# Optimization experiments

Measured on AMD Instinct MI355X. Metric: run time of the kernel, lower is better.

Reference implementation:

```python
import jax, jax.numpy as jnp
import numpy as np

MAX_ITERS = 256  # matches init_kwargs max_iters


def setup_inputs() -> dict:
    key = jax.random.key(0)
    k1, k2 = jax.random.split(key)
    H = W = 4096
    # classic Mandelbrot viewing window
    c_real = jax.random.uniform(k1, (H, W), jnp.float32, -2.0, 0.5)
    c_imag = jax.random.uniform(k2, (H, W), jnp.float32, -1.25, 1.25)
    return {"c_real": c_real, "c_imag": c_imag}


def reference(c_real, c_imag):
    # z starts at c (NOT zero), as in the torch module
    zr0 = c_real
    zi0 = c_imag
    active0 = jnp.ones(c_real.shape, dtype=bool)
    counts0 = jnp.full(c_real.shape, float(MAX_ITERS), dtype=c_real.dtype)

    def body(step, state):
        zr, zi, active, counts = state
        escaped_now = active & (zr * zr + zi * zi >= 4.0)
        counts = jnp.where(escaped_now, step.astype(counts.dtype), counts)
        active = active & ~escaped_now
        # torch loop only updates z for step < max_iters
        do_update = active & (step < MAX_ITERS)
        next_real = zr * zr - zi * zi + c_real
        next_imag = 2.0 * zr * zi + c_imag
        zr = jnp.where(do_update, next_real, zr)
        zi = jnp.where(do_update, next_imag, zi)
        return (zr, zi, active, counts)

    _, _, _, counts = jax.lax.fori_loop(
        0, MAX_ITERS + 1, body, (zr0, zi0, active0, counts0)
    )
    return counts
```

## Files before the change

kernel.cpp:

```cpp
#include <hip/hip_runtime.h>


#define MAX_ITERS 256

typedef __attribute__((ext_vector_type(2))) float f32x2;
typedef __attribute__((ext_vector_type(4))) float f32x4;

__device__ __forceinline__ float mul32(float a, float b) {
    float d; asm("v_mul_f32 %0, %1, %2" : "=v"(d) : "v"(a), "v"(b)); return d;
}
__device__ __forceinline__ float add32(float a, float b) {
    float d; asm("v_add_f32 %0, %1, %2" : "=v"(d) : "v"(a), "v"(b)); return d;
}
__device__ __forceinline__ float fma32(float a, float b, float c) {
    float d; asm("v_fma_f32 %0, %1, %2, %3" : "=v"(d) : "v"(a), "v"(b), "v"(c)); return d;
}
__device__ __forceinline__ float fma32_negc(float a, float b, float c) {
    float d; asm("v_fma_f32 %0, %1, %2, -%3" : "=v"(d) : "v"(a), "v"(b), "v"(c)); return d;
}

__device__ __forceinline__ void iter_checks(float cr, float ci,
                                            float& zr, float& zi,
                                            float& act, float& cnt, int nchecks)
{
    #pragma unroll 8
    for (int s = 0; s < nchecks; ++s) {
        const float zi2 = mul32(zi, zi);
        const float mag = fma32(zr, zr, zi2);
        act = (mag < 4.0f) ? act : 0.0f;
        cnt = cnt + act;
        const float t   = fma32_negc(zr, zr, zi2);
        const float nr  = add32(t, cr);
        const float t2  = add32(zr, zr);
        zi = fma32(t2, zi, ci);
        zr = nr;
    }
}

__device__ __forceinline__ void zstep2(const f32x2 cr, const f32x2 ci,
                                       f32x2& zr, f32x2& zi, f32x2& mag)
{
    f32x2 s, t, u;
    asm("v_pk_mul_f32 %0, %5, %5\n\t"
        "v_pk_fma_f32 %1, %4, %4, %0\n\t"
        "v_pk_fma_f32 %2, %4, %4, %0 neg_lo:[0,0,1] neg_hi:[0,0,1]\n\t"
        "v_pk_add_f32 %3, %4, %4\n\t"
        "v_pk_add_f32 %4, %2, %6\n\t"
        "v_pk_fma_f32 %5, %3, %5, %7"
        : "=&v"(s), "=&v"(mag), "=&v"(t), "=&v"(u), "+v"(zr), "+v"(zi)
        : "v"(cr), "v"(ci));
}

__device__ __forceinline__ void check4(
    const f32x2 crA, const f32x2 ciA, f32x2& zrA, f32x2& ziA,
    const f32x2 crB, const f32x2 ciB, f32x2& zrB, f32x2& ziB,
    float& act0, float& act1, float& act2, float& act3,
    float& cnt0, float& cnt1, float& cnt2, float& cnt3)
{
    f32x2 magA, magB;
    zstep2(crA, ciA, zrA, ziA, magA);
    zstep2(crB, ciB, zrB, ziB, magB);
    act0 = (magA.x < 4.0f) ? act0 : 0.0f;  cnt0 += act0;
    act1 = (magA.y < 4.0f) ? act1 : 0.0f;  cnt1 += act1;
    act2 = (magB.x < 4.0f) ? act2 : 0.0f;  cnt2 += act2;
    act3 = (magB.y < 4.0f) ? act3 : 0.0f;  cnt3 += act3;
}

__device__ __forceinline__ int lane_id() {
    return __builtin_amdgcn_mbcnt_hi(~0u, __builtin_amdgcn_mbcnt_lo(~0u, 0));
}

__device__ __forceinline__ bool in_shortcut(float cr, float ci) {
    const float xq = cr - 0.25f;
    const float q  = xq * xq + ci * ci;
    const bool in_card = (q * (q + xq) - 0.25f * ci * ci) < -1e-3f;
    const float xb = cr + 1.0f;
    const bool in_bulb = (xb * xb + ci * ci) < (0.0625f - 1e-3f);
    return in_card | in_bulb;
}

__global__ void zero_ctrs(unsigned char* ws) {
    if (threadIdx.x < 64)
        *(unsigned*)(ws + (size_t)threadIdx.x * 64u) = 0u;
}

__global__ __launch_bounds__(256) void mandel_stage_a_q(
    const float* __restrict__ c_real, const float* __restrict__ c_imag,
    float* __restrict__ out, unsigned char* __restrict__ ws,
    unsigned seg_cap, int n)
{
    const int tq = blockIdx.x * blockDim.x + threadIdx.x;
    const int p0 = tq << 2;
    if (p0 >= n) return;

    if (p0 + 3 >= n) {
        for (int j = 0; j < 4 && p0 + j < n; ++j) {
            const float cr = c_real[p0 + j], ci = c_imag[p0 + j];
            if (in_shortcut(cr, ci)) { out[p0 + j] = 256.0f; continue; }
            float zr = cr, zi = ci, act = 1.0f, cnt = 0.0f;
            iter_checks(cr, ci, zr, zi, act, cnt, MAX_ITERS);
            out[p0 + j] = cnt;
        }
        return;
    }

    const f32x4 cr4 = *(const f32x4*)(c_real + p0);
    const f32x4 ci4 = *(const f32x4*)(c_imag + p0);
    const f32x2 crA = {cr4.x, cr4.y}, ciA = {ci4.x, ci4.y};
    const f32x2 crB = {cr4.z, cr4.w}, ciB = {ci4.z, ci4.w};
    const bool sc0 = in_shortcut(cr4.x, ci4.x);
    const bool sc1 = in_shortcut(cr4.y, ci4.y);
    const bool sc2 = in_shortcut(cr4.z, ci4.z);
    const bool sc3 = in_shortcut(cr4.w, ci4.w);

    f32x2 zrA = crA, ziA = ciA, zrB = crB, ziB = ciB;
    float act0 = 1.0f, act1 = 1.0f, act2 = 1.0f, act3 = 1.0f;
    float cnt0 = 0.0f, cnt1 = 0.0f, cnt2 = 0.0f, cnt3 = 0.0f;
    #pragma unroll
    for (int s = 0; s < 16; ++s)
        check4(crA, ciA, zrA, ziA, crB, ciB, zrB, ziB,
               act0, act1, act2, act3, cnt0, cnt1, cnt2, cnt3);

    const bool sv0 = (!sc0) && (act0 != 0.0f);
    const bool sv1 = (!sc1) && (act1 != 0.0f);
    const bool sv2 = (!sc2) && (act2 != 0.0f);
    const bool sv3 = (!sc3) && (act3 != 0.0f);

    const unsigned long long m0 = __ballot(sv0);
    const unsigned long long m1 = __ballot(sv1);
    const unsigned long long m2 = __ballot(sv2);
    const unsigned long long m3 = __ballot(sv3);
    const unsigned long long any = m0 | m1 | m2 | m3;
    if (any != 0ull) {
        const int lane = lane_id();
        const int leader = (int)__ffsll(any) - 1;
        const int seg = blockIdx.x & 63;
        unsigned* ctr = (unsigned*)(ws + (size_t)seg * 64u);
        const unsigned c0 = (unsigned)__popcll(m0);
        const unsigned c1 = (unsigned)__popcll(m1);
        const unsigned c2 = (unsigned)__popcll(m2);
        const unsigned c3 = (unsigned)__popcll(m3);
        unsigned base = 0u;
        if (lane == leader) base = atomicAdd(ctr, c0 + c1 + c2 + c3);
        base = (unsigned)__shfl((int)base, leader, 64);
        float4* qf = (float4*)(ws + 4096);
        int*    qi = (int*)(ws + 4096 + (size_t)seg_cap * 64u * 16u);
        const unsigned long long below = (1ull << lane) - 1ull;
        const size_t segbase = (size_t)seg * seg_cap;
        const unsigned pre1 = c0, pre2 = c0 + c1, pre3 = c0 + c1 + c2;

        float zrv[4] = {zrA.x, zrA.y, zrB.x, zrB.y};
        float ziv[4] = {ziA.x, ziA.y, ziB.x, ziB.y};
        float crv[4] = {cr4.x, cr4.y, cr4.z, cr4.w};
        float civ[4] = {ci4.x, ci4.y, ci4.z, ci4.w};
        float cnv[4] = {cnt0, cnt1, cnt2, cnt3};
        const bool svv[4] = {sv0, sv1, sv2, sv3};
        const unsigned prev[4] = {0u, pre1, pre2, pre3};
        const unsigned long long mv[4] = {m0, m1, m2, m3};
        #pragma unroll
        for (int j = 0; j < 4; ++j) {
            if (!svv[j]) continue;
            const unsigned slot = base + prev[j] +
                (unsigned)__popcll(mv[j] & below);
            if (slot < seg_cap) {
                qf[segbase + slot] = make_float4(zrv[j], ziv[j], crv[j], civ[j]);
                qi[segbase + slot] = p0 + j;
            } else {
                float zrs = zrv[j], zis = ziv[j], as = 1.0f, cs = cnv[j];
                iter_checks(crv[j], civ[j], zrs, zis, as, cs, 240);
                out[p0 + j] = cs;
            }
        }
    }
    if (!sv0) out[p0 + 0] = sc0 ? 256.0f : cnt0;
    if (!sv1) out[p0 + 1] = sc1 ? 256.0f : cnt1;
    if (!sv2) out[p0 + 2] = sc2 ? 256.0f : cnt2;
    if (!sv3) out[p0 + 3] = sc3 ? 256.0f : cnt3;
}

__global__ __launch_bounds__(256) void mandel_stage_b_q(
    float* __restrict__ out, const unsigned char* __restrict__ ws,
    unsigned seg_cap, int blocks_per_seg)
{
    const int seg = (int)(blockIdx.x & 63u);
    const int grp = (int)(blockIdx.x >> 6);
    const unsigned cnt_s = *(const unsigned*)(ws + (size_t)seg * 64u);
    const unsigned nq = (cnt_s < seg_cap) ? cnt_s : seg_cap;
    const unsigned q = (nq + 3u) >> 2;
    const unsigned stride = (unsigned)blocks_per_seg * 256u;
    const float4* qf = (const float4*)(ws + 4096);
    const int*    qi = (const int*)(ws + 4096 + (size_t)seg_cap * 64u * 16u);
    const size_t segbase = (size_t)seg * seg_cap;

    for (unsigned k = (unsigned)grp * 256u + threadIdx.x; k < q; k += stride) {
        const unsigned i1 = k + q, i2 = k + 2u * q, i3 = k + 3u * q;
        const bool v1 = (i1 < nq), v2 = (i2 < nq), v3 = (i3 < nq);
        const float4 r0 = qf[segbase + k];
        const float4 r1 = v1 ? qf[segbase + i1] : r0;
        const float4 r2 = v2 ? qf[segbase + i2] : r0;
        const float4 r3 = v3 ? qf[segbase + i3] : r0;
        const int idx0 = qi[segbase + k];
        const int idx1 = v1 ? qi[segbase + i1] : -1;
        const int idx2 = v2 ? qi[segbase + i2] : -1;
        const int idx3 = v3 ? qi[segbase + i3] : -1;

        f32x2 zrA = {r0.x, r1.x}, ziA = {r0.y, r1.y};
        f32x2 crA = {r0.z, r1.z}, ciA = {r0.w, r1.w};
        f32x2 zrB = {r2.x, r3.x}, ziB = {r2.y, r3.y};
        f32x2 crB = {r2.z, r3.z}, ciB = {r2.w, r3.w};
        float act0 = 1.0f, act1 = v1 ? 1.0f : 0.0f;
        float act2 = v2 ? 1.0f : 0.0f, act3 = v3 ? 1.0f : 0.0f;
        float cnt0 = 16.0f, cnt1 = 16.0f, cnt2 = 16.0f, cnt3 = 16.0f;
        #pragma unroll 8
        for (int s = 0; s < 240; ++s)
            check4(crA, ciA, zrA, ziA, crB, ciB, zrB, ziB,
                   act0, act1, act2, act3, cnt0, cnt1, cnt2, cnt3);
        out[idx0] = cnt0;
        if (v1) out[idx1] = cnt1;
        if (v2) out[idx2] = cnt2;
        if (v3) out[idx3] = cnt3;
    }
}

__global__ __launch_bounds__(256) void mandel_mono(
    const float* __restrict__ c_real, const float* __restrict__ c_imag,
    float* __restrict__ out, int n)
{
    int i = blockIdx.x * blockDim.x + threadIdx.x;
    if (i >= n) return;
    const float cr = c_real[i], ci = c_imag[i];
    float zr = cr, zi = ci, act = 1.0f, cnt = 0.0f;
    iter_checks(cr, ci, zr, zi, act, cnt, MAX_ITERS);
    out[i] = cnt;
}

extern "C" void kernel_launch(void* const* d_in, const int* in_sizes, int n_in,
                              void* d_out, int out_size, void* d_ws, size_t ws_size,
                              hipStream_t stream)
{
    const float* c_real = (const float*)d_in[0];
    const float* c_imag = (const float*)d_in[1];
    float* out = (float*)d_out;
    const int n = in_sizes[0];
    const int block = 256;

    unsigned char* ws = (unsigned char*)d_ws;
    const size_t avail = (ws_size > 4096) ? (ws_size - 4096) : 0;
    const unsigned seg_cap = (unsigned)(avail / (64u * 20u));

    if (seg_cap < 8192u) {
        const int gridA = (n + block - 1) / block;
        mandel_mono<<<gridA, block, 0, stream>>>(c_real, c_imag, out, n);
        return;
    }

    zero_ctrs<<<1, 64, 0, stream>>>(ws);

    const int nquads = (n + 3) / 4;
    const int gridA = (nquads + block - 1) / block;
    mandel_stage_a_q<<<gridA, block, 0, stream>>>(c_real, c_imag, out,
                                                  ws, seg_cap, n);
    const int bps = 32;
    mandel_stage_b_q<<<64 * bps, block, 0, stream>>>(out, ws, seg_cap, bps);
}
```

Measured before the change: 237.6 us.

## Split escape-time queue into multi-stage compaction passes with ping-pong buffers

Replaces the single stage-B pass, which runs 240 iterations on every surviving point, with three strip kernels of 40, 80 and 120 iterations. After each strip, points still active are recompacted into a ping-pong queue using wave ballots and per-segment atomic counters. This cuts divergence waste, since each wave in later stages holds only long-lived points. The cost is two extra launches, extra queue reads and writes, and atomics. Counter zeroing also moves from a tiny kernel to hipMemsetAsync.

```diff
diff --git a/kernel.cpp b/kernel.cpp
--- a/kernel.cpp
+++ b/kernel.cpp
@@ -79,20 +79,11 @@
     return in_card | in_bulb;
 }
 
-__global__ void zero_ctrs(unsigned char* ws) {
-    if (threadIdx.x < 64)
-        *(unsigned*)(ws + (size_t)threadIdx.x * 64u) = 0u;
-}
-
-__global__ __launch_bounds__(256) void mandel_stage_a_q(
+__device__ __forceinline__ void phaseA_quad(
     const float* __restrict__ c_real, const float* __restrict__ c_imag,
     float* __restrict__ out, unsigned char* __restrict__ ws,
-    unsigned seg_cap, int n)
-{
-    const int tq = blockIdx.x * blockDim.x + threadIdx.x;
-    const int p0 = tq << 2;
-    if (p0 >= n) return;
-
+    unsigned seg_cap, int n, int p0, int seg)
+{
     if (p0 + 3 >= n) {
         for (int j = 0; j < 4 && p0 + j < n; ++j) {
             const float cr = c_real[p0 + j], ci = c_imag[p0 + j];
@@ -134,20 +125,18 @@
     if (any != 0ull) {
         const int lane = lane_id();
         const int leader = (int)__ffsll(any) - 1;
-        const int seg = blockIdx.x & 63;
         unsigned* ctr = (unsigned*)(ws + (size_t)seg * 64u);
         const unsigned c0 = (unsigned)__popcll(m0);
         const unsigned c1 = (unsigned)__popcll(m1);
         const unsigned c2 = (unsigned)__popcll(m2);
-        const unsigned c3 = (unsigned)__popcll(m3);
         unsigned base = 0u;
-        if (lane == leader) base = atomicAdd(ctr, c0 + c1 + c2 + c3);
+        if (lane == leader)
+            base = atomicAdd(ctr, c0 + c1 + c2 + (unsigned)__popcll(m3));
         base = (unsigned)__shfl((int)base, leader, 64);
         float4* qf = (float4*)(ws + 4096);
         int*    qi = (int*)(ws + 4096 + (size_t)seg_cap * 64u * 16u);
         const unsigned long long below = (1ull << lane) - 1ull;
         const size_t segbase = (size_t)seg * seg_cap;
-        const unsigned pre1 = c0, pre2 = c0 + c1, pre3 = c0 + c1 + c2;
 
         float zrv[4] = {zrA.x, zrA.y, zrB.x, zrB.y};
         float ziv[4] = {ziA.x, ziA.y, ziB.x, ziB.y};
@@ -155,7 +144,7 @@
         float civ[4] = {ci4.x, ci4.y, ci4.z, ci4.w};
         float cnv[4] = {cnt0, cnt1, cnt2, cnt3};
         const bool svv[4] = {sv0, sv1, sv2, sv3};
-        const unsigned prev[4] = {0u, pre1, pre2, pre3};
+        const unsigned prev[4] = {0u, c0, c0 + c1, c0 + c1 + c2};
         const unsigned long long mv[4] = {m0, m1, m2, m3};
         #pragma unroll
         for (int j = 0; j < 4; ++j) {
@@ -178,31 +167,34 @@
     if (!sv3) out[p0 + 3] = sc3 ? 256.0f : cnt3;
 }
 
-__global__ __launch_bounds__(256) void mandel_stage_b_q(
-    float* __restrict__ out, const unsigned char* __restrict__ ws,
-    unsigned seg_cap, int blocks_per_seg)
-{
-    const int seg = (int)(blockIdx.x & 63u);
-    const int grp = (int)(blockIdx.x >> 6);
-    const unsigned cnt_s = *(const unsigned*)(ws + (size_t)seg * 64u);
+template <int NCHECKS, int START, bool HAS_DST>
+__device__ __forceinline__ void strip_phase(
+    float* __restrict__ out, unsigned char* __restrict__ ws,
+    const float4* __restrict__ srcF, const int* __restrict__ srcI,
+    float4* __restrict__ dstF, int* __restrict__ dstI,
+    int src_ctr, int dst_ctr, unsigned seg_cap,
+    int seg, int grp, int blocks_per_seg)
+{
+    const unsigned cnt_s = __hip_atomic_load(
+        (const unsigned*)(ws + (size_t)seg * 64u + (size_t)src_ctr * 4u),
+        __ATOMIC_RELAXED, __HIP_MEMORY_SCOPE_AGENT);
     const unsigned nq = (cnt_s < seg_cap) ? cnt_s : seg_cap;
     const unsigned q = (nq + 3u) >> 2;
     const unsigned stride = (unsigned)blocks_per_seg * 256u;
-    const float4* qf = (const float4*)(ws + 4096);
-    const int*    qi = (const int*)(ws + 4096 + (size_t)seg_cap * 64u * 16u);
     const size_t segbase = (size_t)seg * seg_cap;
+    const int lane = lane_id();
 
     for (unsigned k = (unsigned)grp * 256u + threadIdx.x; k < q; k += stride) {
         const unsigned i1 = k + q, i2 = k + 2u * q, i3 = k + 3u * q;
         const bool v1 = (i1 < nq), v2 = (i2 < nq), v3 = (i3 < nq);
-        const float4 r0 = qf[segbase + k];
-        const float4 r1 = v1 ? qf[segbase + i1] : r0;
-        const float4 r2 = v2 ? qf[segbase + i2] : r0;
-        const float4 r3 = v3 ? qf[segbase + i3] : r0;
-        const int idx0 = qi[segbase + k];
-        const int idx1 = v1 ? qi[segbase + i1] : -1;
-        const int idx2 = v2 ? qi[segbase + i2] : -1;
-        const int idx3 = v3 ? qi[segbase + i3] : -1;
+        const float4 r0 = srcF[segbase + k];
+        const float4 r1 = v1 ? srcF[segbase + i1] : r0;
+        const float4 r2 = v2 ? srcF[segbase + i2] : r0;
+        const float4 r3 = v3 ? srcF[segbase + i3] : r0;
+        const int idx0 = srcI[segbase + k];
+        const int idx1 = v1 ? srcI[segbase + i1] : -1;
+        const int idx2 = v2 ? srcI[segbase + i2] : -1;
+        const int idx3 = v3 ? srcI[segbase + i3] : -1;
 
         f32x2 zrA = {r0.x, r1.x}, ziA = {r0.y, r1.y};
         f32x2 crA = {r0.z, r1.z}, ciA = {r0.w, r1.w};
@@ -210,16 +202,96 @@
         f32x2 crB = {r2.z, r3.z}, ciB = {r2.w, r3.w};
         float act0 = 1.0f, act1 = v1 ? 1.0f : 0.0f;
         float act2 = v2 ? 1.0f : 0.0f, act3 = v3 ? 1.0f : 0.0f;
-        float cnt0 = 16.0f, cnt1 = 16.0f, cnt2 = 16.0f, cnt3 = 16.0f;
+        float cnt0 = (float)START, cnt1 = (float)START;
+        float cnt2 = (float)START, cnt3 = (float)START;
         #pragma unroll 8
-        for (int s = 0; s < 240; ++s)
+        for (int s = 0; s < NCHECKS; ++s)
             check4(crA, ciA, zrA, ziA, crB, ciB, zrB, ziB,
                    act0, act1, act2, act3, cnt0, cnt1, cnt2, cnt3);
-        out[idx0] = cnt0;
-        if (v1) out[idx1] = cnt1;
-        if (v2) out[idx2] = cnt2;
-        if (v3) out[idx3] = cnt3;
-    }
+
+        if (HAS_DST) {
+            const bool sv0 = (act0 != 0.0f);
+            const bool sv1 = (act1 != 0.0f);
+            const bool sv2 = (act2 != 0.0f);
+            const bool sv3 = (act3 != 0.0f);
+            const unsigned long long m0 = __ballot(sv0);
+            const unsigned long long m1 = __ballot(sv1);
+            const unsigned long long m2 = __ballot(sv2);
+            const unsigned long long m3 = __ballot(sv3);
+            const unsigned long long any = m0 | m1 | m2 | m3;
+            if (any != 0ull) {
+                const int leader = (int)__ffsll(any) - 1;
+                unsigned* ctr = (unsigned*)(ws + (size_t)seg * 64u
+                                               + (size_t)dst_ctr * 4u);
+                const unsigned c0 = (unsigned)__popcll(m0);
+                const unsigned c1 = (unsigned)__popcll(m1);
+                const unsigned c2 = (unsigned)__popcll(m2);
+                unsigned base = 0u;
+                if (lane == leader)
+                    base = atomicAdd(ctr, c0 + c1 + c2 + (unsigned)__popcll(m3));
+                base = (unsigned)__shfl((int)base, leader, 64);
+                const unsigned long long below = (1ull << lane) - 1ull;
+
+                float zrv[4] = {zrA.x, zrA.y, zrB.x, zrB.y};
+                float ziv[4] = {ziA.x, ziA.y, ziB.x, ziB.y};
+                float crv[4] = {crA.x, crA.y, crB.x, crB.y};
+                float civ[4] = {ciA.x, ciA.y, ciB.x, ciB.y};
+                float cnv[4] = {cnt0, cnt1, cnt2, cnt3};
+                const int  idxv[4] = {idx0, idx1, idx2, idx3};
+                const bool svv[4] = {sv0, sv1, sv2, sv3};
+                const unsigned prev[4] = {0u, c0, c0 + c1, c0 + c1 + c2};
+                const unsigned long long mv[4] = {m0, m1, m2, m3};
+                #pragma unroll
+                for (int j = 0; j < 4; ++j) {
+                    if (!svv[j]) continue;
+                    const unsigned slot = base + prev[j] +
+                        (unsigned)__popcll(mv[j] & below);
+                    if (slot < seg_cap) {
+                        dstF[segbase + slot] =
+                            make_float4(zrv[j], ziv[j], crv[j], civ[j]);
+                        dstI[segbase + slot] = idxv[j];
+                    } else {
+                        float zrs = zrv[j], zis = ziv[j], as = 1.0f, cs = cnv[j];
+                        iter_checks(crv[j], civ[j], zrs, zis, as, cs,
+                                    256 - START - NCHECKS);
+                        out[idxv[j]] = cs;
+                    }
+                }
+            }
+            if (!sv0) out[idx0] = cnt0;
+            if (v1 && !sv1) out[idx1] = cnt1;
+            if (v2 && !sv2) out[idx2] = cnt2;
+            if (v3 && !sv3) out[idx3] = cnt3;
+        } else {
+            out[idx0] = cnt0;
+            if (v1) out[idx1] = cnt1;
+            if (v2) out[idx2] = cnt2;
+            if (v3) out[idx3] = cnt3;
+        }
+    }
+}
+
+__global__ __launch_bounds__(256) void mandel_stage_a_q(
+    const float* __restrict__ c_real, const float* __restrict__ c_imag,
+    float* __restrict__ out, unsigned char* __restrict__ ws,
+    unsigned seg_cap, int n)
+{
+    const int tq = blockIdx.x * blockDim.x + threadIdx.x;
+    const int p0 = tq << 2;
+    if (p0 >= n) return;
+    phaseA_quad(c_real, c_imag, out, ws, seg_cap, n, p0, blockIdx.x & 63);
+}
+
+template <int NCHECKS, int START, bool HAS_DST>
+__global__ __launch_bounds__(256) void mandel_strip_q(
+    float* __restrict__ out, unsigned char* __restrict__ ws,
+    const float4* __restrict__ srcF, const int* __restrict__ srcI,
+    float4* __restrict__ dstF, int* __restrict__ dstI,
+    int src_ctr, int dst_ctr, unsigned seg_cap, int blocks_per_seg)
+{
+    strip_phase<NCHECKS, START, HAS_DST>(
+        out, ws, srcF, srcI, dstF, dstI, src_ctr, dst_ctr, seg_cap,
+        (int)(blockIdx.x & 63u), (int)(blockIdx.x >> 6), blocks_per_seg);
 }
 
 __global__ __launch_bounds__(256) void mandel_mono(
@@ -246,20 +318,44 @@
 
     unsigned char* ws = (unsigned char*)d_ws;
     const size_t avail = (ws_size > 4096) ? (ws_size - 4096) : 0;
-    const unsigned seg_cap = (unsigned)(avail / (64u * 20u));
-
-    if (seg_cap < 8192u) {
+    const unsigned seg_cap1 = (unsigned)(avail / (64u * 20u));
+    const unsigned seg_cap2 = (unsigned)(avail / (64u * 20u * 2u));
+
+    if (seg_cap1 < 8192u) {
         const int gridA = (n + block - 1) / block;
         mandel_mono<<<gridA, block, 0, stream>>>(c_real, c_imag, out, n);
         return;
     }
 
-    zero_ctrs<<<1, 64, 0, stream>>>(ws);
+    hipMemsetAsync(ws, 0, 4096, stream);
 
     const int nquads = (n + 3) / 4;
     const int gridA = (nquads + block - 1) / block;
+
+    if (seg_cap2 >= 33000u) {
+        const unsigned sc = seg_cap2;
+        float4* q0f = (float4*)(ws + 4096);
+        int*    q0i = (int*)(ws + 4096 + (size_t)sc * 64u * 16u);
+        float4* q1f = (float4*)(ws + 4096 + (size_t)sc * 64u * 20u);
+        int*    q1i = (int*)(ws + 4096 + (size_t)sc * 64u * 20u
+                                       + (size_t)sc * 64u * 16u);
+
+        mandel_stage_a_q<<<gridA, block, 0, stream>>>(c_real, c_imag, out,
+                                                      ws, sc, n);
+        mandel_strip_q<40, 16, true><<<64 * 32, block, 0, stream>>>(
+            out, ws, q0f, q0i, q1f, q1i, 0, 1, sc, 32);
+        mandel_strip_q<80, 56, true><<<64 * 16, block, 0, stream>>>(
+            out, ws, q1f, q1i, q0f, q0i, 1, 2, sc, 16);
+        mandel_strip_q<120, 136, false><<<64 * 16, block, 0, stream>>>(
+            out, ws, q0f, q0i, (float4*)nullptr, (int*)nullptr, 2, 0, sc, 16);
+        return;
+    }
+
     mandel_stage_a_q<<<gridA, block, 0, stream>>>(c_real, c_imag, out,
-                                                  ws, seg_cap, n);
-    const int bps = 32;
-    mandel_stage_b_q<<<64 * bps, block, 0, stream>>>(out, ws, seg_cap, bps);
-}
+                                                  ws, seg_cap1, n);
+    mandel_strip_q<240, 16, false><<<64 * 32, block, 0, stream>>>(
+        out, ws,
+        (const float4*)(ws + 4096),
+        (const int*)(ws + 4096 + (size_t)seg_cap1 * 64u * 16u),
+        (float4*)nullptr, (int*)nullptr, 0, 0, seg_cap1, 32);
+}
```

Measured after the change: 239.0 us. About the same (+0.6%).

## Fuse screening and survivor stages into one persistent kernel with LDS pool

Applied to the files above, without the earlier changes.

Replaces the three-kernel pipeline (counter zeroing, 16-iteration screening with global-memory survivor queues, separate 240-iteration drain kernel) with a single persistent kernel. Each block stages survivors in a shared-memory pool and drains 1024 at a time once the pool fills, then drains the remainder at the end. This removes global queue traffic, global atomics and the extra launches. In exchange it adds block-wide barriers on every group and can leave load imbalance at the tail, since each block's leftover pool is processed by that block alone.

```diff
diff --git a/kernel.cpp b/kernel.cpp
--- a/kernel.cpp
+++ b/kernel.cpp
@@ -2,6 +2,8 @@
 
 
 #define MAX_ITERS 256
+#define POOL_CAP 1280
+#define DRAIN_AT 1024
 
 typedef __attribute__((ext_vector_type(2))) float f32x2;
 typedef __attribute__((ext_vector_type(4))) float f32x4;
@@ -79,159 +81,170 @@
     return in_card | in_bulb;
 }
 
-__global__ void zero_ctrs(unsigned char* ws) {
-    if (threadIdx.x < 64)
-        *(unsigned*)(ws + (size_t)threadIdx.x * 64u) = 0u;
-}
-
-__global__ __launch_bounds__(256) void mandel_stage_a_q(
-    const float* __restrict__ c_real, const float* __restrict__ c_imag,
-    float* __restrict__ out, unsigned char* __restrict__ ws,
-    unsigned seg_cap, int n)
-{
-    const int tq = blockIdx.x * blockDim.x + threadIdx.x;
-    const int p0 = tq << 2;
-    if (p0 >= n) return;
-
-    if (p0 + 3 >= n) {
-        for (int j = 0; j < 4 && p0 + j < n; ++j) {
-            const float cr = c_real[p0 + j], ci = c_imag[p0 + j];
-            if (in_shortcut(cr, ci)) { out[p0 + j] = 256.0f; continue; }
-            float zr = cr, zi = ci, act = 1.0f, cnt = 0.0f;
-            iter_checks(cr, ci, zr, zi, act, cnt, MAX_ITERS);
-            out[p0 + j] = cnt;
-        }
-        return;
-    }
-
-    const f32x4 cr4 = *(const f32x4*)(c_real + p0);
-    const f32x4 ci4 = *(const f32x4*)(c_imag + p0);
-    const f32x2 crA = {cr4.x, cr4.y}, ciA = {ci4.x, ci4.y};
-    const f32x2 crB = {cr4.z, cr4.w}, ciB = {ci4.z, ci4.w};
-    const bool sc0 = in_shortcut(cr4.x, ci4.x);
-    const bool sc1 = in_shortcut(cr4.y, ci4.y);
-    const bool sc2 = in_shortcut(cr4.z, ci4.z);
-    const bool sc3 = in_shortcut(cr4.w, ci4.w);
-
-    f32x2 zrA = crA, ziA = ciA, zrB = crB, ziB = ciB;
-    float act0 = 1.0f, act1 = 1.0f, act2 = 1.0f, act3 = 1.0f;
-    float cnt0 = 0.0f, cnt1 = 0.0f, cnt2 = 0.0f, cnt3 = 0.0f;
-    #pragma unroll
-    for (int s = 0; s < 16; ++s)
+__device__ __forceinline__ void drain4(
+    const float4 r0, const float4 r1, const float4 r2, const float4 r3,
+    const bool v0, const bool v1, const bool v2, const bool v3,
+    const int i0, const int i1, const int i2, const int i3,
+    float* __restrict__ out)
+{
+    f32x2 zrA; zrA.x = r0.x; zrA.y = r1.x;
+    f32x2 ziA; ziA.x = r0.y; ziA.y = r1.y;
+    f32x2 crA; crA.x = r0.z; crA.y = r1.z;
+    f32x2 ciA; ciA.x = r0.w; ciA.y = r1.w;
+    f32x2 zrB; zrB.x = r2.x; zrB.y = r3.x;
+    f32x2 ziB; ziB.x = r2.y; ziB.y = r3.y;
+    f32x2 crB; crB.x = r2.z; crB.y = r3.z;
+    f32x2 ciB; ciB.x = r2.w; ciB.y = r3.w;
+    float act0 = v0 ? 1.0f : 0.0f, act1 = v1 ? 1.0f : 0.0f;
+    float act2 = v2 ? 1.0f : 0.0f, act3 = v3 ? 1.0f : 0.0f;
+    float cnt0 = 16.0f, cnt1 = 16.0f, cnt2 = 16.0f, cnt3 = 16.0f;
+    #pragma unroll 8
+    for (int s = 0; s < 240; ++s)
         check4(crA, ciA, zrA, ziA, crB, ciB, zrB, ziB,
                act0, act1, act2, act3, cnt0, cnt1, cnt2, cnt3);
-
-    const bool sv0 = (!sc0) && (act0 != 0.0f);
-    const bool sv1 = (!sc1) && (act1 != 0.0f);
-    const bool sv2 = (!sc2) && (act2 != 0.0f);
-    const bool sv3 = (!sc3) && (act3 != 0.0f);
-
-    const unsigned long long m0 = __ballot(sv0);
-    const unsigned long long m1 = __ballot(sv1);
-    const unsigned long long m2 = __ballot(sv2);
-    const unsigned long long m3 = __ballot(sv3);
-    const unsigned long long any = m0 | m1 | m2 | m3;
-    if (any != 0ull) {
-        const int lane = lane_id();
-        const int leader = (int)__ffsll(any) - 1;
-        const int seg = blockIdx.x & 63;
-        unsigned* ctr = (unsigned*)(ws + (size_t)seg * 64u);
-        const unsigned c0 = (unsigned)__popcll(m0);
-        const unsigned c1 = (unsigned)__popcll(m1);
-        const unsigned c2 = (unsigned)__popcll(m2);
-        const unsigned c3 = (unsigned)__popcll(m3);
-        unsigned base = 0u;
-        if (lane == leader) base = atomicAdd(ctr, c0 + c1 + c2 + c3);
-        base = (unsigned)__shfl((int)base, leader, 64);
-        float4* qf = (float4*)(ws + 4096);
-        int*    qi = (int*)(ws + 4096 + (size_t)seg_cap * 64u * 16u);
-        const unsigned long long below = (1ull << lane) - 1ull;
-        const size_t segbase = (size_t)seg * seg_cap;
-        const unsigned pre1 = c0, pre2 = c0 + c1, pre3 = c0 + c1 + c2;
-
-        float zrv[4] = {zrA.x, zrA.y, zrB.x, zrB.y};
-        float ziv[4] = {ziA.x, ziA.y, ziB.x, ziB.y};
-        float crv[4] = {cr4.x, cr4.y, cr4.z, cr4.w};
-        float civ[4] = {ci4.x, ci4.y, ci4.z, ci4.w};
-        float cnv[4] = {cnt0, cnt1, cnt2, cnt3};
-        const bool svv[4] = {sv0, sv1, sv2, sv3};
-        const unsigned prev[4] = {0u, pre1, pre2, pre3};
-        const unsigned long long mv[4] = {m0, m1, m2, m3};
-        #pragma unroll
-        for (int j = 0; j < 4; ++j) {
-            if (!svv[j]) continue;
-            const unsigned slot = base + prev[j] +
-                (unsigned)__popcll(mv[j] & below);
-            if (slot < seg_cap) {
-                qf[segbase + slot] = make_float4(zrv[j], ziv[j], crv[j], civ[j]);
-                qi[segbase + slot] = p0 + j;
+    if (v0) out[i0] = cnt0;
+    if (v1) out[i1] = cnt1;
+    if (v2) out[i2] = cnt2;
+    if (v3) out[i3] = cnt3;
+}
+
+__global__ __launch_bounds__(256) void mandel_fused(
+    const float* __restrict__ c_real, const float* __restrict__ c_imag,
+    float* __restrict__ out, int n)
+{
+    __shared__ float4 poolF[POOL_CAP];
+    __shared__ int    poolI[POOL_CAP];
+    __shared__ int    pool_cnt;
+
+    const int tid = (int)threadIdx.x;
+    const int lane = lane_id();
+    if (tid == 0) pool_cnt = 0;
+    __syncthreads();
+
+    const int ngroups = (n + 1023) >> 10;
+
+    for (int g = (int)blockIdx.x; g < ngroups; g += (int)gridDim.x) {
+        const int p0 = (g << 10) + (tid << 2);
+        if (p0 < n) {
+            if (p0 + 3 >= n) {
+                for (int j = 0; j < 4 && p0 + j < n; ++j) {
+                    const float cr = c_real[p0 + j], ci = c_imag[p0 + j];
+                    if (in_shortcut(cr, ci)) { out[p0 + j] = 256.0f; continue; }
+                    float zr = cr, zi = ci, act = 1.0f, cnt = 0.0f;
+                    iter_checks(cr, ci, zr, zi, act, cnt, MAX_ITERS);
+                    out[p0 + j] = cnt;
+                }
             } else {
-                float zrs = zrv[j], zis = ziv[j], as = 1.0f, cs = cnv[j];
-                iter_checks(crv[j], civ[j], zrs, zis, as, cs, 240);
-                out[p0 + j] = cs;
+                const f32x4 cr4 = *(const f32x4*)(c_real + p0);
+                const f32x4 ci4 = *(const f32x4*)(c_imag + p0);
+                f32x2 crA; crA.x = cr4.x; crA.y = cr4.y;
+                f32x2 ciA; ciA.x = ci4.x; ciA.y = ci4.y;
+                f32x2 crB; crB.x = cr4.z; crB.y = cr4.w;
+                f32x2 ciB; ciB.x = ci4.z; ciB.y = ci4.w;
+                const bool sc0 = in_shortcut(cr4.x, ci4.x);
+                const bool sc1 = in_shortcut(cr4.y, ci4.y);
+                const bool sc2 = in_shortcut(cr4.z, ci4.z);
+                const bool sc3 = in_shortcut(cr4.w, ci4.w);
+
+                f32x2 zrA = crA, ziA = ciA, zrB = crB, ziB = ciB;
+                float act0 = 1.0f, act1 = 1.0f, act2 = 1.0f, act3 = 1.0f;
+                float cnt0 = 0.0f, cnt1 = 0.0f, cnt2 = 0.0f, cnt3 = 0.0f;
+                #pragma unroll
+                for (int s = 0; s < 16; ++s)
+                    check4(crA, ciA, zrA, ziA, crB, ciB, zrB, ziB,
+                           act0, act1, act2, act3, cnt0, cnt1, cnt2, cnt3);
+
+                const bool sv0 = (!sc0) && (act0 != 0.0f);
+                const bool sv1 = (!sc1) && (act1 != 0.0f);
+                const bool sv2 = (!sc2) && (act2 != 0.0f);
+                const bool sv3 = (!sc3) && (act3 != 0.0f);
+
+                const unsigned long long m0 = __ballot(sv0);
+                const unsigned long long m1 = __ballot(sv1);
+                const unsigned long long m2 = __ballot(sv2);
+                const unsigned long long m3 = __ballot(sv3);
+                const unsigned long long any = m0 | m1 | m2 | m3;
+                if (any != 0ull) {
+                    const int leader = (int)__ffsll(any) - 1;
+                    const unsigned c0 = (unsigned)__popcll(m0);
+                    const unsigned c1 = (unsigned)__popcll(m1);
+                    const unsigned c2 = (unsigned)__popcll(m2);
+                    int base_i = 0;
+                    if (lane == leader)
+                        base_i = atomicAdd(&pool_cnt,
+                            (int)(c0 + c1 + c2 + (unsigned)__popcll(m3)));
+                    const unsigned base =
+                        (unsigned)__shfl(base_i, leader, 64);
+                    const unsigned long long below = (1ull << lane) - 1ull;
+
+                    const float zrv[4] = {zrA.x, zrA.y, zrB.x, zrB.y};
+                    const float ziv[4] = {ziA.x, ziA.y, ziB.x, ziB.y};
+                    const float crv[4] = {cr4.x, cr4.y, cr4.z, cr4.w};
+                    const float civ[4] = {ci4.x, ci4.y, ci4.z, ci4.w};
+                    const float cnv[4] = {cnt0, cnt1, cnt2, cnt3};
+                    const bool svv[4] = {sv0, sv1, sv2, sv3};
+                    const unsigned prev[4] = {0u, c0, c0 + c1, c0 + c1 + c2};
+                    const unsigned long long mv[4] = {m0, m1, m2, m3};
+                    #pragma unroll
+                    for (int j = 0; j < 4; ++j) {
+                        if (!svv[j]) continue;
+                        const unsigned slot = base + prev[j] +
+                            (unsigned)__popcll(mv[j] & below);
+                        if (slot < POOL_CAP) {
+                            poolF[slot] = make_float4(zrv[j], ziv[j],
+                                                      crv[j], civ[j]);
+                            poolI[slot] = p0 + j;
+                        } else {
+                            float zrs = zrv[j], zis = ziv[j];
+                            float as = 1.0f, cs = cnv[j];
+                            iter_checks(crv[j], civ[j], zrs, zis, as, cs, 240);
+                            out[p0 + j] = cs;
+                        }
+                    }
+                }
+                if (!sv0) out[p0 + 0] = sc0 ? 256.0f : cnt0;
+                if (!sv1) out[p0 + 1] = sc1 ? 256.0f : cnt1;
+                if (!sv2) out[p0 + 2] = sc2 ? 256.0f : cnt2;
+                if (!sv3) out[p0 + 3] = sc3 ? 256.0f : cnt3;
             }
         }
+        __syncthreads();
+        const int cnt = pool_cnt;
+        if (cnt >= DRAIN_AT) {
+            const float4 r0 = poolF[tid];
+            const float4 r1 = poolF[tid + 256];
+            const float4 r2 = poolF[tid + 512];
+            const float4 r3 = poolF[tid + 768];
+            const int i0 = poolI[tid];
+            const int i1 = poolI[tid + 256];
+            const int i2 = poolI[tid + 512];
+            const int i3 = poolI[tid + 768];
+            __syncthreads();
+            const int eff = (cnt < POOL_CAP) ? cnt : POOL_CAP;
+            for (int t = tid; t < eff - DRAIN_AT; t += 256) {
+                poolF[t] = poolF[DRAIN_AT + t];
+                poolI[t] = poolI[DRAIN_AT + t];
+            }
+            if (tid == 0) pool_cnt = eff - DRAIN_AT;
+            drain4(r0, r1, r2, r3, true, true, true, true,
+                   i0, i1, i2, i3, out);
+        }
+        __syncthreads();
     }
-    if (!sv0) out[p0 + 0] = sc0 ? 256.0f : cnt0;
-    if (!sv1) out[p0 + 1] = sc1 ? 256.0f : cnt1;
-    if (!sv2) out[p0 + 2] = sc2 ? 256.0f : cnt2;
-    if (!sv3) out[p0 + 3] = sc3 ? 256.0f : cnt3;
-}
-
-__global__ __launch_bounds__(256) void mandel_stage_b_q(
-    float* __restrict__ out, const unsigned char* __restrict__ ws,
-    unsigned seg_cap, int blocks_per_seg)
-{
-    const int seg = (int)(blockIdx.x & 63u);
-    const int grp = (int)(blockIdx.x >> 6);
-    const unsigned cnt_s = *(const unsigned*)(ws + (size_t)seg * 64u);
-    const unsigned nq = (cnt_s < seg_cap) ? cnt_s : seg_cap;
-    const unsigned q = (nq + 3u) >> 2;
-    const unsigned stride = (unsigned)blocks_per_seg * 256u;
-    const float4* qf = (const float4*)(ws + 4096);
-    const int*    qi = (const int*)(ws + 4096 + (size_t)seg_cap * 64u * 16u);
-    const size_t segbase = (size_t)seg * seg_cap;
-
-    for (unsigned k = (unsigned)grp * 256u + threadIdx.x; k < q; k += stride) {
-        const unsigned i1 = k + q, i2 = k + 2u * q, i3 = k + 3u * q;
-        const bool v1 = (i1 < nq), v2 = (i2 < nq), v3 = (i3 < nq);
-        const float4 r0 = qf[segbase + k];
-        const float4 r1 = v1 ? qf[segbase + i1] : r0;
-        const float4 r2 = v2 ? qf[segbase + i2] : r0;
-        const float4 r3 = v3 ? qf[segbase + i3] : r0;
-        const int idx0 = qi[segbase + k];
-        const int idx1 = v1 ? qi[segbase + i1] : -1;
-        const int idx2 = v2 ? qi[segbase + i2] : -1;
-        const int idx3 = v3 ? qi[segbase + i3] : -1;
-
-        f32x2 zrA = {r0.x, r1.x}, ziA = {r0.y, r1.y};
-        f32x2 crA = {r0.z, r1.z}, ciA = {r0.w, r1.w};
-        f32x2 zrB = {r2.x, r3.x}, ziB = {r2.y, r3.y};
-        f32x2 crB = {r2.z, r3.z}, ciB = {r2.w, r3.w};
-        float act0 = 1.0f, act1 = v1 ? 1.0f : 0.0f;
-        float act2 = v2 ? 1.0f : 0.0f, act3 = v3 ? 1.0f : 0.0f;
-        float cnt0 = 16.0f, cnt1 = 16.0f, cnt2 = 16.0f, cnt3 = 16.0f;
-        #pragma unroll 8
-        for (int s = 0; s < 240; ++s)
-            check4(crA, ciA, zrA, ziA, crB, ciB, zrB, ziB,
-                   act0, act1, act2, act3, cnt0, cnt1, cnt2, cnt3);
-        out[idx0] = cnt0;
-        if (v1) out[idx1] = cnt1;
-        if (v2) out[idx2] = cnt2;
-        if (v3) out[idx3] = cnt3;
+
+    int cnt = pool_cnt;
+    if (cnt > POOL_CAP) cnt = POOL_CAP;
+    const int i0 = tid, i1 = tid + 256, i2 = tid + 512, i3 = tid + 768;
+    const bool v0 = i0 < cnt, v1 = i1 < cnt, v2 = i2 < cnt, v3 = i3 < cnt;
+    if (v0 | v1 | v2 | v3) {
+        const float4 r0 = v0 ? poolF[i0] : make_float4(0.f, 0.f, 0.f, 0.f);
+        const float4 r1 = v1 ? poolF[i1] : r0;
+        const float4 r2 = v2 ? poolF[i2] : r0;
+        const float4 r3 = v3 ? poolF[i3] : r0;
+        drain4(r0, r1, r2, r3, v0, v1, v2, v3,
+               v0 ? poolI[i0] : 0, v1 ? poolI[i1] : 0,
+               v2 ? poolI[i2] : 0, v3 ? poolI[i3] : 0, out);
     }
-}
-
-__global__ __launch_bounds__(256) void mandel_mono(
-    const float* __restrict__ c_real, const float* __restrict__ c_imag,
-    float* __restrict__ out, int n)
-{
-    int i = blockIdx.x * blockDim.x + threadIdx.x;
-    if (i >= n) return;
-    const float cr = c_real[i], ci = c_imag[i];
-    float zr = cr, zi = ci, act = 1.0f, cnt = 0.0f;
-    iter_checks(cr, ci, zr, zi, act, cnt, MAX_ITERS);
-    out[i] = cnt;
 }
 
 extern "C" void kernel_launch(void* const* d_in, const int* in_sizes, int n_in,
@@ -242,24 +255,9 @@
     const float* c_imag = (const float*)d_in[1];
     float* out = (float*)d_out;
     const int n = in_sizes[0];
-    const int block = 256;
-
-    unsigned char* ws = (unsigned char*)d_ws;
-    const size_t avail = (ws_size > 4096) ? (ws_size - 4096) : 0;
-    const unsigned seg_cap = (unsigned)(avail / (64u * 20u));
-
-    if (seg_cap < 8192u) {
-        const int gridA = (n + block - 1) / block;
-        mandel_mono<<<gridA, block, 0, stream>>>(c_real, c_imag, out, n);
-        return;
-    }
-
-    zero_ctrs<<<1, 64, 0, stream>>>(ws);
-
-    const int nquads = (n + 3) / 4;
-    const int gridA = (nquads + block - 1) / block;
-    mandel_stage_a_q<<<gridA, block, 0, stream>>>(c_real, c_imag, out,
-                                                  ws, seg_cap, n);
-    const int bps = 32;
-    mandel_stage_b_q<<<64 * bps, block, 0, stream>>>(out, ws, seg_cap, bps);
-}
+
+    const int ngroups = (n + 1023) >> 10;
+    int grid = 1536;
+    if (grid > ngroups) grid = (ngroups > 0) ? ngroups : 1;
+    mandel_fused<<<grid, 256, 0, stream>>>(c_real, c_imag, out, n);
+}
```

New measurement: 237.1 us. About the same (-0.2%).
